# Optimization experiments

Hardware: AMD Instinct MI355X
Metric: run time of the kernel (lower is better)

The kernel has to match this reference:

```python
import jax, jax.numpy as jnp
import numpy as np

S = 8192      # sequence length
E = 1024      # embeddingDimension
D = 64        # linearDimension


def setup_inputs() -> dict:
    key = jax.random.key(0)
    ks = jax.random.split(key, 9)
    lim = 1.0 / np.sqrt(E)
    inp = {
        "x": jax.random.normal(ks[0], (S, E), dtype=jnp.float32),
        "y": jax.random.normal(ks[1], (S, E), dtype=jnp.float32),
        "z": jax.random.normal(ks[2], (S, E), dtype=jnp.float32),
        "Wq": jax.random.uniform(ks[3], (E, D), jnp.float32, -lim, lim),
        "bq": jax.random.uniform(ks[4], (D,), jnp.float32, -lim, lim),
        "Wk": jax.random.uniform(ks[5], (E, D), jnp.float32, -lim, lim),
        "bk": jax.random.uniform(ks[6], (D,), jnp.float32, -lim, lim),
        "Wv": jax.random.uniform(ks[7], (E, D), jnp.float32, -lim, lim),
        "bv": jax.random.uniform(ks[8], (D,), jnp.float32, -lim, lim),
    }
    return inp


def reference(x, y, z, Wq, bq, Wk, bk, Wv, bv):
    q = x @ Wq + bq                      # [S, D]
    k = y @ Wk + bk                      # [S, D]
    v = z @ Wv + bv                      # [S, D]
    scores = q @ k.T                     # [S, S]
    n = scores.shape[0]
    # masked=True: add triu(-inf, diag=1) causal mask (faithful to torch.triu of a full -inf matrix)
    neg_inf = jnp.float32(-jnp.inf)
    causal = jnp.triu(jnp.full((n, n), neg_inf, dtype=scores.dtype), k=1)
    scores = scores + causal
    # original scales by sqrt(size(0)) = sqrt(seq_len), softmax over last dim (torch 2D default)
    attn = jax.nn.softmax(scores / jnp.sqrt(jnp.float32(n)), axis=-1)
    return attn @ v                      # [S, D]
```

## Files before the change

### kernel.cpp

```cpp
#include <hip/hip_runtime.h>

#define SEQ 8192
#define EMB 1024
#define DIM 64

typedef __attribute__((ext_vector_type(8))) short bf16x8;
typedef __attribute__((ext_vector_type(4))) float f32x4;
typedef __attribute__((ext_vector_type(16))) float f32x16;

#if __has_builtin(__builtin_amdgcn_exp2f)
#define EXP2 __builtin_amdgcn_exp2f
#else
#define EXP2 exp2f
#endif

#define SCL 0.0159396779f

__device__ inline unsigned short f2bf(float f) {
    union { float f; unsigned u; } x; x.f = f;
    unsigned r = x.u + 0x7FFFu + ((x.u >> 16) & 1u);
    return (unsigned short)(r >> 16);
}

__device__ inline unsigned cvtpk(float lo, float hi) {
    unsigned r;
    asm("v_cvt_pk_bf16_f32 %0, %1, %2" : "=v"(r) : "v"(lo), "v"(hi));
    return r;
}

__device__ __forceinline__ void gload16(const float* g, float* l) {
    __builtin_amdgcn_global_load_lds(
        (const __attribute__((address_space(1))) unsigned*)g,
        (__attribute__((address_space(3))) unsigned*)l, 16, 0, 0);
}


__global__ __launch_bounds__(256) void wt_kernel(
    const float* __restrict__ Wq, const float* __restrict__ Wk,
    const float* __restrict__ Wv, unsigned short* __restrict__ Wt)
{
    __shared__ float L[64][65];

    const int b   = (int)blockIdx.x;
    const int mat = b >> 4;
    const int kt  = b & 15;
    const float* W = (mat == 0) ? Wq : (mat == 1) ? Wk : Wv;
    const int tid = (int)threadIdx.x;

    const float* src = W + (size_t)kt * 64 * DIM;
    #pragma unroll
    for (int i = 0; i < 16; ++i) {
        const int idx = i * 256 + tid;
        L[idx >> 6][idx & 63] = src[idx];
    }
    __syncthreads();

    unsigned short* dst = Wt + (size_t)(mat * 32 + kt * 2) * 2048;
    #pragma unroll
    for (int h = 0; h < 2; ++h) {
        const int s = tid * 16 + h * 8;
        const int sgo   = s >> 11;
        const int wcg   = (s >> 9) & 3;
        const int lanep = (s >> 3) & 63;
        const int qq = lanep >> 4, c = lanep & 15;
        const int kb = sgo * 32 + qq * 8;
        const int n  = wcg * 16 + c;
        uint4 w4;
        w4.x = cvtpk(L[kb + 0][n], L[kb + 1][n]);
        w4.y = cvtpk(L[kb + 2][n], L[kb + 3][n]);
        w4.z = cvtpk(L[kb + 4][n], L[kb + 5][n]);
        w4.w = cvtpk(L[kb + 6][n], L[kb + 7][n]);
        *(uint4*)&dst[s] = w4;
    }
}

__device__ inline bf16x8 cvt8(float4 a, float4 b) {
    union { unsigned u[4]; bf16x8 v; } r;
    r.u[0] = cvtpk(a.x, a.y);
    r.u[1] = cvtpk(a.z, a.w);
    r.u[2] = cvtpk(b.x, b.y);
    r.u[3] = cvtpk(b.z, b.w);
    return r.v;
}

__global__ __launch_bounds__(256) void proj_kernel(
    const float* __restrict__ x, const float* __restrict__ y, const float* __restrict__ z,
    const float* __restrict__ bq, const float* __restrict__ bk, const float* __restrict__ bv,
    const unsigned short* __restrict__ Wt, unsigned short* __restrict__ qkv)
{
    __shared__ float pool[12288];

    const int bid = (int)blockIdx.x;
    const int mat = bid >> 8;
    const int rb  = (bid & 255) * 32;

    const int tid  = (int)threadIdx.x;
    const int lane = tid & 63;
    const int w    = tid >> 6;
    const int wr   = w & 1;
    const int kh   = w >> 1;
    const int c    = lane & 15;
    const int qq   = lane >> 4;

    const float* X  = (mat == 0) ? x  : (mat == 1) ? y  : z;
    const float* Bv = (mat == 0) ? bq : (mat == 1) ? bk : bv;
    const unsigned short* Wm = Wt + (size_t)mat * 65536;
    unsigned short* outp = qkv + (size_t)mat * (SEQ * DIM);

    float* poolw = pool + w * 3072;
    const float* Xw = X + (size_t)(rb + wr * 16) * EMB + kh * 512;

    f32x4 acc[4];
    #pragma unroll
    for (int i = 0; i < 4; ++i) acc[i] = (f32x4){0.f, 0.f, 0.f, 0.f};

    bf16x8 wreg[3][8];

    #define STAGE(buf, t)                                                       \
        {                                                                       \
            const int k0_ = (t) * 64;                                           \
            _Pragma("unroll")                                                   \
            for (int j = 0; j < 4; ++j) {                                       \
                const int rloc = j * 4 + qq;                                    \
                const int g = c ^ (rloc & 7);                                   \
                gload16(Xw + (size_t)rloc * EMB + k0_ + g * 4,                  \
                        poolw + (buf) * 1024 + j * 256);                        \
            }                                                                   \
        }
    #define WLOAD(slot, t)                                                      \
        {                                                                       \
            const int sgb = kh * 16 + (t) * 2;                                  \
            _Pragma("unroll")                                                   \
            for (int ks2 = 0; ks2 < 2; ++ks2)                                   \
                _Pragma("unroll")                                               \
                for (int wc2 = 0; wc2 < 4; ++wc2)                               \
                    wreg[slot][ks2 * 4 + wc2] = *(const bf16x8*)(Wm +           \
                        ((size_t)((sgb + ks2) * 4 + wc2) * 64 + lane) * 8);     \
        }
    #define COMP(bt)                                                            \
        {                                                                       \
            const float* rowb = poolw + (bt) * 1024 + c * 64;                   \
            _Pragma("unroll")                                                   \
            for (int ks2 = 0; ks2 < 2; ++ks2) {                                 \
                float4 fa = *(const float4*)(rowb +                             \
                                (((ks2 * 8 + qq * 2)     ^ (c & 7)) << 2));     \
                float4 fb = *(const float4*)(rowb +                             \
                                (((ks2 * 8 + qq * 2 + 1) ^ (c & 7)) << 2));     \
                bf16x8 af = cvt8(fa, fb);                                       \
                _Pragma("unroll")                                               \
                for (int wc2 = 0; wc2 < 4; ++wc2)                               \
                    acc[wc2] = __builtin_amdgcn_mfma_f32_16x16x32_bf16(         \
                        af, wreg[bt][ks2 * 4 + wc2], acc[wc2], 0, 0, 0);        \
            }                                                                   \
        }

    STAGE(0, 0); WLOAD(0, 0);
    asm volatile("" ::: "memory");
    STAGE(1, 1); WLOAD(1, 1);
    asm volatile("" ::: "memory");
    STAGE(2, 2); WLOAD(2, 2);

    #pragma unroll
    for (int t = 0; t < 8; ++t) {
        if (t <= 5)      asm volatile("s_waitcnt vmcnt(24)" ::: "memory");
        else if (t == 6) asm volatile("s_waitcnt vmcnt(12)" ::: "memory");
        else             asm volatile("s_waitcnt vmcnt(0)"  ::: "memory");
        COMP(t % 3);
        if (t < 5) { STAGE(t % 3, t + 3); WLOAD(t % 3, t + 3); }
    }
    #undef STAGE
    #undef WLOAD
    #undef COMP

    __syncthreads();
    float (*part)[32][68] = (float (*)[32][68])pool;
    #pragma unroll
    for (int wc2 = 0; wc2 < 4; ++wc2)
        #pragma unroll
        for (int i = 0; i < 4; ++i)
            part[kh][wr * 16 + qq * 4 + i][wc2 * 16 + c] = acc[wc2][i];
    __syncthreads();

    const int T = rb >> 5;
    if (mat == 0) {
        const int row = tid >> 3;
        const int c0  = (tid & 7) * 8;
        float v[8];
        #pragma unroll
        for (int j = 0; j < 8; ++j)
            v[j] = part[0][row][c0 + j] + part[1][row][c0 + j] + Bv[c0 + j];
        uint4 pk4;
        pk4.x = cvtpk(v[0], v[1]); pk4.y = cvtpk(v[2], v[3]);
        pk4.z = cvtpk(v[4], v[5]); pk4.w = cvtpk(v[6], v[7]);
        *(uint4*)&outp[(size_t)(rb + row) * DIM + c0] = pk4;
    } else if (mat == 1) {
        const int ks2 = tid >> 6;
        const int hi2 = (tid >> 5) & 1;
        const int col = tid & 31;
        const int d0  = ks2 * 16 + hi2 * 8;
        float v[8];
        #pragma unroll
        for (int j = 0; j < 8; ++j)
            v[j] = part[0][col][d0 + j] + part[1][col][d0 + j] + Bv[d0 + j];
        uint4 pk4;
        pk4.x = cvtpk(v[0], v[1]); pk4.y = cvtpk(v[2], v[3]);
        pk4.z = cvtpk(v[4], v[5]); pk4.w = cvtpk(v[6], v[7]);
        *(uint4*)&outp[(size_t)T * 2048 + tid * 8] = pk4;
    } else {
        const int i2  = tid >> 7;
        const int h   = (tid >> 6) & 1;
        const int hi2 = (tid >> 5) & 1;
        const int col = tid & 31;
        const int r0  = i2 * 16 + hi2 * 8;
        const int cv  = h * 32 + col;
        const float bb = Bv[cv];
        float v[8];
        #pragma unroll
        for (int j = 0; j < 8; ++j)
            v[j] = part[0][r0 + j][cv] + part[1][r0 + j][cv] + bb;
        uint4 pk4;
        pk4.x = cvtpk(v[0], v[1]); pk4.y = cvtpk(v[2], v[3]);
        pk4.z = cvtpk(v[4], v[5]); pk4.w = cvtpk(v[6], v[7]);
        *(uint4*)&outp[(size_t)T * 2048 + tid * 8] = pk4;
    }
}

__global__ __launch_bounds__(256, 3) void attn_kernel(
    const unsigned short* __restrict__ qkv, float* __restrict__ out,
    float* __restrict__ Opart, float* __restrict__ MLpart)
{
    const unsigned short* Q  = qkv;
    const unsigned short* KF = qkv + SEQ * DIM;
    const unsigned short* VF = qkv + 2 * SEQ * DIM;

    __shared__ float Oall[4][32][68];
    __shared__ float Ml[4][32][2];
    __shared__ float sScl[4][32];
    __shared__ float sM[32];
    __shared__ float sL[32];

    const int u = 1151 - (int)blockIdx.x;
    int g;
    if (u < 32) g = 0; else if (u < 96) g = 1; else if (u < 192) g = 2;
    else if (u < 320) g = 3; else if (u < 480) g = 4; else if (u < 672) g = 5;
    else if (u < 896) g = 6; else g = 7;
    const int o_  = u - 16 * g * (g + 1);
    const int qt  = 32 * g + o_ / (g + 1);
    const int cid = o_ - (o_ / (g + 1)) * (g + 1);

    const int m0 = qt * 32;
    const int tid = (int)threadIdx.x;
    const int lane = tid & 63;
    const int w = tid >> 6;
    const int col = lane & 31;
    const int hi = lane >> 5;

    bf16x8 qf[4];
    {
        const unsigned short* Qr = Q + (size_t)(m0 + col) * DIM + hi * 8;
        #pragma unroll
        for (int ks = 0; ks < 4; ++ks) qf[ks] = *(const bf16x8*)(Qr + ks * 16);
    }

    f32x16 o0, o1;
    #pragma unroll
    for (int r = 0; r < 16; ++r) { o0[r] = 0.f; o1[r] = 0.f; }
    float m_i = -1e30f, l_i = 0.f;

    const int nT = qt + 1;
    const int tb = cid * 32;
    const int te = (tb + 32 < nT) ? (tb + 32) : nT;
    const int nC = te - tb;
    const int w0 = tb + ((nC * w) >> 2);
    const int w1 = tb + ((nC * (w + 1)) >> 2);
    const int nW = w1 - w0;
    const int nP = nW >> 1;

    bf16x8 kA[4], kB[4];
    if (nP > 0) {
        const unsigned short* kb0 = KF + (size_t)w0 * 2048 + (size_t)lane * 8;
        #pragma unroll
        for (int ks = 0; ks < 4; ++ks) kA[ks] = *(const bf16x8*)(kb0 + ks * 512);
        #pragma unroll
        for (int ks = 0; ks < 4; ++ks) kB[ks] = *(const bf16x8*)(kb0 + 2048 + ks * 512);
    }

    for (int pi = 0; pi < nP; ++pi) {
        const int t = w0 + 2 * pi;

        f32x16 sa, sb;
        #pragma unroll
        for (int r = 0; r < 16; ++r) { sa[r] = 0.f; sb[r] = 0.f; }
        __builtin_amdgcn_s_setprio(1);
        #pragma unroll
        for (int ks = 0; ks < 4; ++ks) {
            sa = __builtin_amdgcn_mfma_f32_32x32x16_bf16(kA[ks], qf[ks], sa, 0, 0, 0);
            sb = __builtin_amdgcn_mfma_f32_32x32x16_bf16(kB[ks], qf[ks], sb, 0, 0, 0);
        }
        __builtin_amdgcn_s_setprio(0);

        if (pi + 1 < nP) {
            const unsigned short* kbn = KF + (size_t)(t + 2) * 2048 + (size_t)lane * 8;
            #pragma unroll
            for (int ks = 0; ks < 4; ++ks) kA[ks] = *(const bf16x8*)(kbn + ks * 512);
            #pragma unroll
            for (int ks = 0; ks < 4; ++ks) kB[ks] = *(const bf16x8*)(kbn + 2048 + ks * 512);
        }

        const unsigned short* vb_ = VF + (size_t)t * 2048 + (size_t)lane * 8;
        bf16x8 va[4], vbf[4];
        #pragma unroll
        for (int i = 0; i < 4; ++i) va[i]  = *(const bf16x8*)(vb_ + i * 1024);
        #pragma unroll
        for (int i = 0; i < 4; ++i) vbf[i] = *(const bf16x8*)(vb_ + 512 + i * 1024);

        float p0[16], p1[16];
        #pragma unroll
        for (int r = 0; r < 16; ++r) { p0[r] = sa[r] * SCL; p1[r] = sb[r] * SCL; }
        if (t + 1 == qt) {
            #pragma unroll
            for (int r = 0; r < 16; ++r) {
                const int kvr = (r & 3) + 8 * (r >> 2) + 4 * hi;
                if (kvr > col) p1[r] = -1e30f;
            }
        }
        float tm = fmaxf(p0[0], p1[0]);
        #pragma unroll
        for (int r = 1; r < 16; ++r) tm = fmaxf(tm, fmaxf(p0[r], p1[r]));
        tm = fmaxf(tm, __shfl_xor(tm, 32));
        if (!__all(tm <= m_i + 2.0f)) {
            const float mn = fmaxf(m_i, tm);
            const float alpha = EXP2(m_i - mn);
            m_i = mn;
            l_i *= alpha;
            #pragma unroll
            for (int r = 0; r < 16; ++r) { o0[r] *= alpha; o1[r] *= alpha; }
        }
        float rs = 0.f;
        #pragma unroll
        for (int r = 0; r < 16; ++r) { p0[r] = EXP2(p0[r] - m_i); rs += p0[r]; }
        #pragma unroll
        for (int r = 0; r < 16; ++r) { p1[r] = EXP2(p1[r] - m_i); rs += p1[r]; }
        rs += __shfl_xor(rs, 32);
        l_i += rs;

        unsigned pwA[8], pwB[8];
        #pragma unroll
        for (int i = 0; i < 8; ++i) pwA[i] = cvtpk(p0[2 * i], p0[2 * i + 1]);
        #pragma unroll
        for (int i = 0; i < 8; ++i) pwB[i] = cvtpk(p1[2 * i], p1[2 * i + 1]);
        asm volatile("v_permlane32_swap_b32 %0, %1" : "+v"(pwA[0]), "+v"(pwA[2]));
        asm volatile("v_permlane32_swap_b32 %0, %1" : "+v"(pwA[1]), "+v"(pwA[3]));
        asm volatile("v_permlane32_swap_b32 %0, %1" : "+v"(pwA[4]), "+v"(pwA[6]));
        asm volatile("v_permlane32_swap_b32 %0, %1" : "+v"(pwA[5]), "+v"(pwA[7]));
        asm volatile("v_permlane32_swap_b32 %0, %1" : "+v"(pwB[0]), "+v"(pwB[2]));
        asm volatile("v_permlane32_swap_b32 %0, %1" : "+v"(pwB[1]), "+v"(pwB[3]));
        asm volatile("v_permlane32_swap_b32 %0, %1" : "+v"(pwB[4]), "+v"(pwB[6]));
        asm volatile("v_permlane32_swap_b32 %0, %1" : "+v"(pwB[5]), "+v"(pwB[7]));
        union { unsigned uu[4]; bf16x8 v; } pa0, pa1, pb0, pb1;
        pa0.uu[0] = pwA[0]; pa0.uu[1] = pwA[1]; pa0.uu[2] = pwA[2]; pa0.uu[3] = pwA[3];
        pa1.uu[0] = pwA[4]; pa1.uu[1] = pwA[5]; pa1.uu[2] = pwA[6]; pa1.uu[3] = pwA[7];
        pb0.uu[0] = pwB[0]; pb0.uu[1] = pwB[1]; pb0.uu[2] = pwB[2]; pb0.uu[3] = pwB[3];
        pb1.uu[0] = pwB[4]; pb1.uu[1] = pwB[5]; pb1.uu[2] = pwB[6]; pb1.uu[3] = pwB[7];

        __builtin_amdgcn_s_setprio(1);
        o0 = __builtin_amdgcn_mfma_f32_32x32x16_bf16(va[0],  pa0.v, o0, 0, 0, 0);
        o1 = __builtin_amdgcn_mfma_f32_32x32x16_bf16(vbf[0], pa0.v, o1, 0, 0, 0);
        o0 = __builtin_amdgcn_mfma_f32_32x32x16_bf16(va[1],  pa1.v, o0, 0, 0, 0);
        o1 = __builtin_amdgcn_mfma_f32_32x32x16_bf16(vbf[1], pa1.v, o1, 0, 0, 0);
        o0 = __builtin_amdgcn_mfma_f32_32x32x16_bf16(va[2],  pb0.v, o0, 0, 0, 0);
        o1 = __builtin_amdgcn_mfma_f32_32x32x16_bf16(vbf[2], pb0.v, o1, 0, 0, 0);
        o0 = __builtin_amdgcn_mfma_f32_32x32x16_bf16(va[3],  pb1.v, o0, 0, 0, 0);
        o1 = __builtin_amdgcn_mfma_f32_32x32x16_bf16(vbf[3], pb1.v, o1, 0, 0, 0);
        __builtin_amdgcn_s_setprio(0);
    }

    if (nW & 1) {
        const int t = w1 - 1;
        const unsigned short* kb = KF + (size_t)t * 2048 + (size_t)lane * 8;
        const unsigned short* vb_ = VF + (size_t)t * 2048 + (size_t)lane * 8;
        bf16x8 kT[4];
        #pragma unroll
        for (int ks = 0; ks < 4; ++ks) kT[ks] = *(const bf16x8*)(kb + ks * 512);
        bf16x8 va0 = *(const bf16x8*)(vb_);
        bf16x8 va1 = *(const bf16x8*)(vb_ + 1024);
        bf16x8 vb0 = *(const bf16x8*)(vb_ + 512);
        bf16x8 vb1 = *(const bf16x8*)(vb_ + 1536);

        f32x16 sa;
        #pragma unroll
        for (int r = 0; r < 16; ++r) sa[r] = 0.f;
        __builtin_amdgcn_s_setprio(1);
        #pragma unroll
        for (int ks = 0; ks < 4; ++ks)
            sa = __builtin_amdgcn_mfma_f32_32x32x16_bf16(kT[ks], qf[ks], sa, 0, 0, 0);
        __builtin_amdgcn_s_setprio(0);

        float p0[16];
        #pragma unroll
        for (int r = 0; r < 16; ++r) p0[r] = sa[r] * SCL;
        if (t == qt) {
            #pragma unroll
            for (int r = 0; r < 16; ++r) {
                const int kvr = (r & 3) + 8 * (r >> 2) + 4 * hi;
                if (kvr > col) p0[r] = -1e30f;
            }
        }
        float tm = p0[0];
        #pragma unroll
        for (int r = 1; r < 16; ++r) tm = fmaxf(tm, p0[r]);
        tm = fmaxf(tm, __shfl_xor(tm, 32));
        if (!__all(tm <= m_i + 2.0f)) {
            const float mn = fmaxf(m_i, tm);
            const float alpha = EXP2(m_i - mn);
            m_i = mn;
            l_i *= alpha;
            #pragma unroll
            for (int r = 0; r < 16; ++r) { o0[r] *= alpha; o1[r] *= alpha; }
        }
        float rs = 0.f;
        #pragma unroll
        for (int r = 0; r < 16; ++r) { p0[r] = EXP2(p0[r] - m_i); rs += p0[r]; }
        rs += __shfl_xor(rs, 32);
        l_i += rs;

        unsigned pwA[8];
        #pragma unroll
        for (int i = 0; i < 8; ++i) pwA[i] = cvtpk(p0[2 * i], p0[2 * i + 1]);
        asm volatile("v_permlane32_swap_b32 %0, %1" : "+v"(pwA[0]), "+v"(pwA[2]));
        asm volatile("v_permlane32_swap_b32 %0, %1" : "+v"(pwA[1]), "+v"(pwA[3]));
        asm volatile("v_permlane32_swap_b32 %0, %1" : "+v"(pwA[4]), "+v"(pwA[6]));
        asm volatile("v_permlane32_swap_b32 %0, %1" : "+v"(pwA[5]), "+v"(pwA[7]));
        union { unsigned uu[4]; bf16x8 v; } pa0, pa1;
        pa0.uu[0] = pwA[0]; pa0.uu[1] = pwA[1]; pa0.uu[2] = pwA[2]; pa0.uu[3] = pwA[3];
        pa1.uu[0] = pwA[4]; pa1.uu[1] = pwA[5]; pa1.uu[2] = pwA[6]; pa1.uu[3] = pwA[7];

        __builtin_amdgcn_s_setprio(1);
        o0 = __builtin_amdgcn_mfma_f32_32x32x16_bf16(va0, pa0.v, o0, 0, 0, 0);
        o1 = __builtin_amdgcn_mfma_f32_32x32x16_bf16(vb0, pa0.v, o1, 0, 0, 0);
        o0 = __builtin_amdgcn_mfma_f32_32x32x16_bf16(va1, pa1.v, o0, 0, 0, 0);
        o1 = __builtin_amdgcn_mfma_f32_32x32x16_bf16(vb1, pa1.v, o1, 0, 0, 0);
        __builtin_amdgcn_s_setprio(0);
    }

    #pragma unroll
    for (int r = 0; r < 16; ++r) {
        const int d = (r & 3) + 8 * (r >> 2) + 4 * hi;
        Oall[w][col][d]      = o0[r];
        Oall[w][col][32 + d] = o1[r];
    }
    if (hi == 0) { Ml[w][col][0] = m_i; Ml[w][col][1] = l_i; }
    __syncthreads();

    if (tid < 32) {
        float M = Ml[0][tid][0];
        #pragma unroll
        for (int w2 = 1; w2 < 4; ++w2) M = fmaxf(M, Ml[w2][tid][0]);
        float L = 0.f;
        #pragma unroll
        for (int w2 = 0; w2 < 4; ++w2) {
            const float sc = EXP2(Ml[w2][tid][0] - M);
            sScl[w2][tid] = sc;
            L += Ml[w2][tid][1] * sc;
        }
        sM[tid] = M;
        sL[tid] = L;
    }
    __syncthreads();

    const int r = tid >> 3;
    const int c0 = (tid & 7) * 8;
    f32x4 a0 = (f32x4){0.f, 0.f, 0.f, 0.f};
    f32x4 a1 = (f32x4){0.f, 0.f, 0.f, 0.f};
    #pragma unroll
    for (int w2 = 0; w2 < 4; ++w2) {
        const float sc = sScl[w2][r];
        const float* Orow = &Oall[w2][r][c0];
        a0 += (*(const f32x4*)(Orow)) * sc;
        a1 += (*(const f32x4*)(Orow + 4)) * sc;
    }
    if (qt < 32) {
        const float inv = 1.f / sL[r];
        float* op = out + (size_t)(m0 + r) * DIM + c0;
        *(f32x4*)(op)     = a0 * inv;
        *(f32x4*)(op + 4) = a1 * inv;
    } else {
        const int pb = 16 * (g - 1) * (g + 2) + (qt - 32 * g) * (g + 1) + cid;
        float* op = Opart + (size_t)pb * 2048 + r * 64 + c0;
        *(f32x4*)(op)     = a0;
        *(f32x4*)(op + 4) = a1;
        if (tid < 32) {
            MLpart[(size_t)pb * 64 + tid * 2]     = sM[tid];
            MLpart[(size_t)pb * 64 + tid * 2 + 1] = sL[tid];
        }
    }
}

__global__ __launch_bounds__(256) void fixup_kernel(
    const float* __restrict__ Opart, const float* __restrict__ MLpart,
    float* __restrict__ out)
{
    __shared__ float sScl[8][32];
    __shared__ float sInvL[32];

    const int qt = 32 + (int)blockIdx.x;
    const int g  = qt >> 5;
    const int nc = g + 1;
    const int pb = 16 * (g - 1) * (g + 2) + (qt - 32 * g) * nc;
    const int tid = (int)threadIdx.x;

    if (tid < 32) {
        float M = -1e30f;
        for (int c2 = 0; c2 < nc; ++c2)
            M = fmaxf(M, MLpart[(size_t)(pb + c2) * 64 + tid * 2]);
        float L = 0.f;
        for (int c2 = 0; c2 < nc; ++c2) {
            const float sc = EXP2(MLpart[(size_t)(pb + c2) * 64 + tid * 2] - M);
            sScl[c2][tid] = sc;
            L += MLpart[(size_t)(pb + c2) * 64 + tid * 2 + 1] * sc;
        }
        sInvL[tid] = 1.f / L;
    }
    __syncthreads();

    const int r = tid >> 3;
    const int c0 = (tid & 7) * 8;
    f32x4 a0 = (f32x4){0.f, 0.f, 0.f, 0.f};
    f32x4 a1 = (f32x4){0.f, 0.f, 0.f, 0.f};
    for (int c2 = 0; c2 < nc; ++c2) {
        const float sc = sScl[c2][r];
        const float* Op = Opart + (size_t)(pb + c2) * 2048 + r * 64 + c0;
        a0 += (*(const f32x4*)(Op)) * sc;
        a1 += (*(const f32x4*)(Op + 4)) * sc;
    }
    const float inv = sInvL[r];
    float* op = out + (size_t)(qt * 32 + r) * DIM + c0;
    *(f32x4*)(op)     = a0 * inv;
    *(f32x4*)(op + 4) = a1 * inv;
}

extern "C" void kernel_launch(void* const* d_in, const int* in_sizes, int n_in,
                              void* d_out, int out_size, void* d_ws, size_t ws_size,
                              hipStream_t stream) {
    const float* x  = (const float*)d_in[0];
    const float* y  = (const float*)d_in[1];
    const float* z  = (const float*)d_in[2];
    const float* Wq = (const float*)d_in[3];
    const float* bq = (const float*)d_in[4];
    const float* Wk = (const float*)d_in[5];
    const float* bk = (const float*)d_in[6];
    const float* Wv = (const float*)d_in[7];
    const float* bv = (const float*)d_in[8];

    unsigned short* qkv = (unsigned short*)d_ws;
    unsigned short* Wt  = (unsigned short*)((char*)d_ws + 3145728);
    float* Opart        = (float*)((char*)d_ws + 3538944);
    float* MLpart       = (float*)((char*)d_ws + 12713984);
    float* out          = (float*)d_out;

    hipLaunchKernelGGL(wt_kernel,    dim3(48),   dim3(256), 0, stream, Wq, Wk, Wv, Wt);
    hipLaunchKernelGGL(proj_kernel,  dim3(768),  dim3(256), 0, stream, x, y, z, bq, bk, bv, Wt, qkv);
    hipLaunchKernelGGL(attn_kernel,  dim3(1152), dim3(256), 0, stream, qkv, out, Opart, MLpart);
    hipLaunchKernelGGL(fixup_kernel, dim3(224),  dim3(256), 0, stream, Opart, MLpart, out);
}
```

Before: 54.40 us.

## Split projection into 16-row blocks with four-way K split across waves

The projection kernel now gives each block 16 rows instead of 32, and each of its four waves handles a quarter of the embedding dimension instead of a 2x2 row/K split. This doubles the grid to 1536 blocks, halves shared memory per block, and adds an occupancy hint of four blocks per CU. The aim is more parallelism and occupancy for the memory-bound x/y/z read. In exchange the epilogue reduces four partial sums and writes narrower 8-byte stores into the K/V tiled layouts. The weight register loads per block are also duplicated across twice as many blocks.

```diff
diff --git a/kernel.cpp b/kernel.cpp
--- a/kernel.cpp
+++ b/kernel.cpp
@@ -83,22 +83,20 @@
     return r.v;
 }
 
-__global__ __launch_bounds__(256) void proj_kernel(
+__global__ __launch_bounds__(256, 4) void proj_kernel(
     const float* __restrict__ x, const float* __restrict__ y, const float* __restrict__ z,
     const float* __restrict__ bq, const float* __restrict__ bk, const float* __restrict__ bv,
     const unsigned short* __restrict__ Wt, unsigned short* __restrict__ qkv)
 {
-    __shared__ float pool[12288];
+    __shared__ float pool[6144];
 
     const int bid = (int)blockIdx.x;
-    const int mat = bid >> 8;
-    const int rb  = (bid & 255) * 32;
+    const int mat = bid >> 9;
+    const int rb  = (bid & 511) * 16;
 
     const int tid  = (int)threadIdx.x;
     const int lane = tid & 63;
-    const int w    = tid >> 6;
-    const int wr   = w & 1;
-    const int kh   = w >> 1;
+    const int kq   = tid >> 6;
     const int c    = lane & 15;
     const int qq   = lane >> 4;
 
@@ -107,51 +105,44 @@
     const unsigned short* Wm = Wt + (size_t)mat * 65536;
     unsigned short* outp = qkv + (size_t)mat * (SEQ * DIM);
 
-    float* poolw = pool + w * 3072;
-    const float* Xw = X + (size_t)(rb + wr * 16) * EMB + kh * 512;
+    float* poolw = pool + kq * 1536;
+    const float* Xw = X + (size_t)rb * EMB + kq * 256;
 
     f32x4 acc[4];
     #pragma unroll
     for (int i = 0; i < 4; ++i) acc[i] = (f32x4){0.f, 0.f, 0.f, 0.f};
 
-    bf16x8 wreg[3][8];
+    bf16x8 wreg[3][4];
 
     #define STAGE(buf, t)                                                       \
         {                                                                       \
-            const int k0_ = (t) * 64;                                           \
+            const int k0_ = (t) * 32;                                           \
             _Pragma("unroll")                                                   \
-            for (int j = 0; j < 4; ++j) {                                       \
-                const int rloc = j * 4 + qq;                                    \
-                const int g = c ^ (rloc & 7);                                   \
+            for (int j = 0; j < 2; ++j) {                                       \
+                const int rloc = j * 8 + (lane >> 3);                           \
+                const int g = (lane & 7) ^ (rloc & 7);                          \
                 gload16(Xw + (size_t)rloc * EMB + k0_ + g * 4,                  \
-                        poolw + (buf) * 1024 + j * 256);                        \
+                        poolw + (buf) * 512 + j * 256);                         \
             }                                                                   \
         }
     #define WLOAD(slot, t)                                                      \
         {                                                                       \
-            const int sgb = kh * 16 + (t) * 2;                                  \
+            const int sg_ = kq * 8 + (t);                                       \
             _Pragma("unroll")                                                   \
-            for (int ks2 = 0; ks2 < 2; ++ks2)                                   \
-                _Pragma("unroll")                                               \
-                for (int wc2 = 0; wc2 < 4; ++wc2)                               \
-                    wreg[slot][ks2 * 4 + wc2] = *(const bf16x8*)(Wm +           \
-                        ((size_t)((sgb + ks2) * 4 + wc2) * 64 + lane) * 8);     \
+            for (int wc2 = 0; wc2 < 4; ++wc2)                                   \
+                wreg[slot][wc2] = *(const bf16x8*)(Wm +                         \
+                    ((size_t)(sg_ * 4 + wc2) * 64 + lane) * 8);                 \
         }
     #define COMP(bt)                                                            \
         {                                                                       \
-            const float* rowb = poolw + (bt) * 1024 + c * 64;                   \
+            const float* rowb = poolw + (bt) * 512 + c * 32;                    \
+            float4 fa = *(const float4*)(rowb + (((qq * 2)     ^ (c & 7)) << 2)); \
+            float4 fb = *(const float4*)(rowb + (((qq * 2 + 1) ^ (c & 7)) << 2)); \
+            bf16x8 af = cvt8(fa, fb);                                           \
             _Pragma("unroll")                                                   \
-            for (int ks2 = 0; ks2 < 2; ++ks2) {                                 \
-                float4 fa = *(const float4*)(rowb +                             \
-                                (((ks2 * 8 + qq * 2)     ^ (c & 7)) << 2));     \
-                float4 fb = *(const float4*)(rowb +                             \
-                                (((ks2 * 8 + qq * 2 + 1) ^ (c & 7)) << 2));     \
-                bf16x8 af = cvt8(fa, fb);                                       \
-                _Pragma("unroll")                                               \
-                for (int wc2 = 0; wc2 < 4; ++wc2)                               \
-                    acc[wc2] = __builtin_amdgcn_mfma_f32_16x16x32_bf16(         \
-                        af, wreg[bt][ks2 * 4 + wc2], acc[wc2], 0, 0, 0);        \
-            }                                                                   \
+            for (int wc2 = 0; wc2 < 4; ++wc2)                                   \
+                acc[wc2] = __builtin_amdgcn_mfma_f32_16x16x32_bf16(             \
+                    af, wreg[bt][wc2], acc[wc2], 0, 0, 0);                      \
         }
 
     STAGE(0, 0); WLOAD(0, 0);
@@ -162,8 +153,8 @@
 
     #pragma unroll
     for (int t = 0; t < 8; ++t) {
-        if (t <= 5)      asm volatile("s_waitcnt vmcnt(24)" ::: "memory");
-        else if (t == 6) asm volatile("s_waitcnt vmcnt(12)" ::: "memory");
+        if (t <= 5)      asm volatile("s_waitcnt vmcnt(12)" ::: "memory");
+        else if (t == 6) asm volatile("s_waitcnt vmcnt(6)"  ::: "memory");
         else             asm volatile("s_waitcnt vmcnt(0)"  ::: "memory");
         COMP(t % 3);
         if (t < 5) { STAGE(t % 3, t + 3); WLOAD(t % 3, t + 3); }
@@ -173,55 +164,61 @@
     #undef COMP
 
     __syncthreads();
-    float (*part)[32][68] = (float (*)[32][68])pool;
+    float (*part)[16][68] = (float (*)[16][68])pool;
     #pragma unroll
     for (int wc2 = 0; wc2 < 4; ++wc2)
         #pragma unroll
         for (int i = 0; i < 4; ++i)
-            part[kh][wr * 16 + qq * 4 + i][wc2 * 16 + c] = acc[wc2][i];
+            part[kq][qq * 4 + i][wc2 * 16 + c] = acc[wc2][i];
     __syncthreads();
 
-    const int T = rb >> 5;
+    const int T2 = rb >> 5;
+    const int cb = rb & 31;
     if (mat == 0) {
-        const int row = tid >> 3;
-        const int c0  = (tid & 7) * 8;
-        float v[8];
-        #pragma unroll
-        for (int j = 0; j < 8; ++j)
-            v[j] = part[0][row][c0 + j] + part[1][row][c0 + j] + Bv[c0 + j];
-        uint4 pk4;
-        pk4.x = cvtpk(v[0], v[1]); pk4.y = cvtpk(v[2], v[3]);
-        pk4.z = cvtpk(v[4], v[5]); pk4.w = cvtpk(v[6], v[7]);
-        *(uint4*)&outp[(size_t)(rb + row) * DIM + c0] = pk4;
+        const int row = tid >> 4;
+        const int c0  = (tid & 15) * 4;
+        float v0 = part[0][row][c0+0] + part[1][row][c0+0] + part[2][row][c0+0] + part[3][row][c0+0] + Bv[c0+0];
+        float v1 = part[0][row][c0+1] + part[1][row][c0+1] + part[2][row][c0+1] + part[3][row][c0+1] + Bv[c0+1];
+        float v2 = part[0][row][c0+2] + part[1][row][c0+2] + part[2][row][c0+2] + part[3][row][c0+2] + Bv[c0+2];
+        float v3 = part[0][row][c0+3] + part[1][row][c0+3] + part[2][row][c0+3] + part[3][row][c0+3] + Bv[c0+3];
+        uint2 pk;
+        pk.x = cvtpk(v0, v1); pk.y = cvtpk(v2, v3);
+        *(uint2*)&outp[(size_t)(rb + row) * DIM + c0] = pk;
     } else if (mat == 1) {
-        const int ks2 = tid >> 6;
+        const int ks  = tid >> 7;
+        const int ks2 = (tid >> 7) & 1;
+        const int kss = tid >> 7;
+        (void)ks; (void)ks2; (void)kss;
+        const int jh = tid & 1;
+        const int cl = (tid >> 1) & 15;
         const int hi2 = (tid >> 5) & 1;
-        const int col = tid & 31;
-        const int d0  = ks2 * 16 + hi2 * 8;
-        float v[8];
-        #pragma unroll
-        for (int j = 0; j < 8; ++j)
-            v[j] = part[0][col][d0 + j] + part[1][col][d0 + j] + Bv[d0 + j];
-        uint4 pk4;
-        pk4.x = cvtpk(v[0], v[1]); pk4.y = cvtpk(v[2], v[3]);
-        pk4.z = cvtpk(v[4], v[5]); pk4.w = cvtpk(v[6], v[7]);
-        *(uint4*)&outp[(size_t)T * 2048 + tid * 8] = pk4;
+        const int ksf = tid >> 6;
+        const int d0 = ksf * 16 + hi2 * 8 + jh * 4;
+        float v0 = part[0][cl][d0+0] + part[1][cl][d0+0] + part[2][cl][d0+0] + part[3][cl][d0+0] + Bv[d0+0];
+        float v1 = part[0][cl][d0+1] + part[1][cl][d0+1] + part[2][cl][d0+1] + part[3][cl][d0+1] + Bv[d0+1];
+        float v2 = part[0][cl][d0+2] + part[1][cl][d0+2] + part[2][cl][d0+2] + part[3][cl][d0+2] + Bv[d0+2];
+        float v3 = part[0][cl][d0+3] + part[1][cl][d0+3] + part[2][cl][d0+3] + part[3][cl][d0+3] + Bv[d0+3];
+        const size_t base = ((size_t)(T2 * 4 + ksf) * 2 + hi2) * 256 + (size_t)(cb + cl) * 8 + jh * 4;
+        uint2 pk;
+        pk.x = cvtpk(v0, v1); pk.y = cvtpk(v2, v3);
+        *(uint2*)&outp[base] = pk;
     } else {
-        const int i2  = tid >> 7;
-        const int h   = (tid >> 6) & 1;
-        const int hi2 = (tid >> 5) & 1;
-        const int col = tid & 31;
-        const int r0  = i2 * 16 + hi2 * 8;
+        const int jh  = tid & 1;
+        const int col = (tid >> 1) & 31;
+        const int hi2 = (tid >> 6) & 1;
+        const int h   = tid >> 7;
+        const int i2  = cb >> 4;
         const int cv  = h * 32 + col;
         const float bb = Bv[cv];
-        float v[8];
-        #pragma unroll
-        for (int j = 0; j < 8; ++j)
-            v[j] = part[0][r0 + j][cv] + part[1][r0 + j][cv] + bb;
-        uint4 pk4;
-        pk4.x = cvtpk(v[0], v[1]); pk4.y = cvtpk(v[2], v[3]);
-        pk4.z = cvtpk(v[4], v[5]); pk4.w = cvtpk(v[6], v[7]);
-        *(uint4*)&outp[(size_t)T * 2048 + tid * 8] = pk4;
+        const int r0 = hi2 * 8 + jh * 4;
+        float v0 = part[0][r0+0][cv] + part[1][r0+0][cv] + part[2][r0+0][cv] + part[3][r0+0][cv] + bb;
+        float v1 = part[0][r0+1][cv] + part[1][r0+1][cv] + part[2][r0+1][cv] + part[3][r0+1][cv] + bb;
+        float v2 = part[0][r0+2][cv] + part[1][r0+2][cv] + part[2][r0+2][cv] + part[3][r0+2][cv] + bb;
+        float v3 = part[0][r0+3][cv] + part[1][r0+3][cv] + part[2][r0+3][cv] + part[3][r0+3][cv] + bb;
+        const size_t base = ((size_t)(T2 * 2 + i2) * 2 + h) * 512 + (size_t)(hi2 * 32 + col) * 8 + jh * 4;
+        uint2 pk;
+        pk.x = cvtpk(v0, v1); pk.y = cvtpk(v2, v3);
+        *(uint2*)&outp[base] = pk;
     }
 }
 
@@ -559,7 +556,7 @@
     float* out          = (float*)d_out;
 
     hipLaunchKernelGGL(wt_kernel,    dim3(48),   dim3(256), 0, stream, Wq, Wk, Wv, Wt);
-    hipLaunchKernelGGL(proj_kernel,  dim3(768),  dim3(256), 0, stream, x, y, z, bq, bk, bv, Wt, qkv);
+    hipLaunchKernelGGL(proj_kernel,  dim3(1536), dim3(256), 0, stream, x, y, z, bq, bk, bv, Wt, qkv);
     hipLaunchKernelGGL(attn_kernel,  dim3(1152), dim3(256), 0, stream, qkv, out, Opart, MLpart);
     hipLaunchKernelGGL(fixup_kernel, dim3(224),  dim3(256), 0, stream, Opart, MLpart, out);
 }
```

Result: no change. 54.17 us (-0.4%).
